# Kernel tuning notes

Hardware: AMD Instinct MI355X
Metric: run time of the kernel (lower is better)

The kernel has to match this reference:

```python
import jax, jax.numpy as jnp
import numpy as np

N, P, S, ENT = 256, 4, 40, 60
E = 1 + P + S + ENT          # 105 graph nodes (query + paras + sents + ents)
D = 1024                     # input_dim == hidden_dim
H, T = 8, 3                  # gnn heads, edge types
DH = D // H                  # per-head output dim
NEG = -1e30


def setup_inputs() -> dict:
    key = jax.random.key(0)
    ks = jax.random.split(key, 12)
    f = lambda k, sh, s: jax.random.normal(k, sh, jnp.float32) * s
    return {
        "query_vec": f(ks[0], (N, D), 1.0),
        "para_state": f(ks[1], (N, P, D), 1.0),
        "sent_state": f(ks[2], (N, S, D), 1.0),
        "ent_state": f(ks[3], (N, ENT, D), 1.0),
        "para_mask": jax.random.randint(ks[4], (N, P), 0, 2).astype(jnp.float32),
        "sent_mask": jax.random.randint(ks[5], (N, S), 0, 2).astype(jnp.float32),
        "ent_mask": jax.random.randint(ks[6], (N, ENT), 0, 2).astype(jnp.float32),
        "adj": jax.random.randint(ks[7], (N, E, E), 0, T + 1).astype(jnp.int32),
        "W": f(ks[8], (H, T, D, DH), 0.05),        # per head/edge-type projection
        "a": f(ks[9], (H, T, 2 * DH), 0.05),       # GAT attention vector [a1;a2]
        "qW1": f(ks[10], (H, T, D, 2 * DH), 0.05), # query-gate layer 1
        "qW2": f(ks[11], (H, T, 2 * DH, 2 * DH), 0.05),  # query-gate layer 2
    }


def _graph_block(x, query_vec, node_mask, adj, W, a, qW1, qW2):
    # x: [N,E,D], node_mask: [N,E,1], adj: [N,E,E] int (0 = no edge, 1..T = edge type)
    # per head/edge-type projections: [H,T,N,E,DH]
    h = jnp.einsum('ned,htdk->htnek', x, W)
    # query-conditioned gate (q_attn=True): sigmoid(relu(q @ W1) @ W2) -> [H,T,N,2DH]
    g = jax.nn.sigmoid(jnp.einsum('htnk,htkm->htnm',
                                  jax.nn.relu(jnp.einsum('nd,htdk->htnk', query_vec, qW1)),
                                  qW2))
    # decomposed GAT score: score[i,j] = lrelu((g1*h_i)@a1 + (g2*h_j)@a2)
    a1, a2 = a[..., :DH], a[..., DH:]
    f1 = jnp.einsum('htnek,htnk->htne', h, g[..., :DH] * a1[:, :, None, :])
    f2 = jnp.einsum('htnek,htnk->htne', h, g[..., DH:] * a2[:, :, None, :])
    score = jax.nn.leaky_relu(f1[..., :, None] + f2[..., None, :], 0.2)  # [H,T,N,E,E]
    # accumulate only where adj matches the edge type (i+1)
    etype = (jnp.arange(T, dtype=adj.dtype) + 1)[None, :, None, None, None]
    scores = jnp.sum(jnp.where(adj[None, None] == etype, score, 0.0), axis=1)  # [H,N,E,E]
    scores = jnp.where(adj[None] > 0, scores, NEG)
    coefs = jax.nn.softmax(scores, axis=-1)                 # [H,N,E,E]
    # original uses the last edge-type projection, node-masked, for aggregation
    h_last = h[:, -1] * node_mask[None]                     # [H,N,E,DH]
    out = jnp.einsum('hnij,hnjd->hnid', coefs, h_last)      # [H,N,E,DH]
    out = jnp.transpose(out, (1, 2, 0, 3)).reshape(x.shape[0], E, H * DH)
    out = jax.nn.relu(out)                                  # dropout p=0 in eval
    return out + x                                          # residual (identity align)


def reference(query_vec, para_state, sent_state, ent_state,
              para_mask, sent_mask, ent_mask, adj, W, a, qW1, qW2):
    x = jnp.concatenate([query_vec[:, None, :], para_state, sent_state, ent_state], axis=1)  # [N,E,D]
    node_mask = jnp.concatenate(
        [jnp.ones((x.shape[0], 1), x.dtype), para_mask, sent_mask, ent_mask], axis=-1)[..., None]  # [N,E,1]
    graph_state = _graph_block(x, query_vec, node_mask, adj, W, a, qW1, qW2)  # [N,E,D]
    return graph_state
```

## Files before the change

### kernel.cpp

```cpp
#include <hip/hip_runtime.h>
#include <stdint.h>


typedef unsigned short u16;
typedef __bf16 bf16;
typedef __bf16 bf16x8 __attribute__((ext_vector_type(8)));
typedef float f32x4 __attribute__((ext_vector_type(4)));

#define N_ 256
#define E_ 105
#define D_ 1024
#define H_ 8
#define DH_ 128
#define NE_ 26880

__device__ __forceinline__ u16 f2b(float f) { bf16 h = (bf16)f; return __builtin_bit_cast(u16, h); }
__device__ __forceinline__ float b2f(u16 u) { bf16 h = __builtin_bit_cast(bf16, u); return (float)h; }

#define AS1 __attribute__((address_space(1)))
#define AS3 __attribute__((address_space(3)))

__device__ __forceinline__ void load16_lds(const void* g, void* l) {
  __builtin_amdgcn_global_load_lds((AS1 void*)(unsigned long long)(uintptr_t)g,
                                   (AS3 void*)l, 16, 0, 0);
}

__device__ __forceinline__ void gemm128(u16* lds, const u16* A, const u16* B, int K,
                                        int lda, int ldb, f32x4 (&acc)[4][4]) {
  u16* lA = lds;
  u16* lB = lds + 8192;
  const int tid  = threadIdx.x;
  const int lane = tid & 63;
  const int wave = tid >> 6;
  const int ln15 = lane & 15;
  const int lq   = lane >> 4;
  const int wRow = (wave >> 1) * 64;
  const int wCol = (wave & 1) * 64;

  const int iters = K >> 6;
  for (int kt = 0; kt < iters; ++kt) {
    const char* Ab = (const char*)A + kt * 128;
    const char* Bb = (const char*)B + kt * 128;
#pragma unroll
    for (int m = 0; m < 4; ++m) {
      int ci  = m * 256 + tid;
      int row = ci >> 3;
      int g   = (ci & 7) ^ (row & 7);
      char* dstA = (char*)lA + m * 4096 + wave * 1024;
      char* dstB = (char*)lB + m * 4096 + wave * 1024;
      load16_lds(Ab + (long)row * ((long)lda * 2) + g * 16, dstA);
      load16_lds(Bb + (long)row * ((long)ldb * 2) + g * 16, dstB);
    }
    __syncthreads();
#pragma unroll
    for (int ks = 0; ks < 2; ++ks) {
      const int cc = ks * 4 + lq;
      bf16x8 af[4], bfv[4];
#pragma unroll
      for (int i = 0; i < 4; ++i) {
        int r = wRow + i * 16 + ln15;
        af[i] = *(const bf16x8*)&lA[r * 64 + ((cc ^ (r & 7)) << 3)];
        int c = wCol + i * 16 + ln15;
        bfv[i] = *(const bf16x8*)&lB[c * 64 + ((cc ^ (c & 7)) << 3)];
      }
#pragma unroll
      for (int i = 0; i < 4; ++i)
#pragma unroll
        for (int j = 0; j < 4; ++j)
          acc[i][j] = __builtin_amdgcn_mfma_f32_16x16x32_bf16(af[i], bfv[j], acc[i][j], 0, 0, 0);
    }
    __syncthreads();
  }
}

__device__ __forceinline__ void zero_acc(f32x4 (&acc)[4][4]) {
  f32x4 z = {0.f, 0.f, 0.f, 0.f};
#pragma unroll
  for (int i = 0; i < 4; ++i)
#pragma unroll
    for (int j = 0; j < 4; ++j) acc[i][j] = z;
}

__device__ __forceinline__ void tr_tile(const float* src, u16* dst, int R, int C,
                                        long sStr, long dStr, int bz, int bxy,
                                        u16 (*t)[33], int tid) {
  const int tilesC = C >> 5;
  const int tr = (bxy / tilesC) << 5;
  const int tc = (bxy % tilesC) << 5;
  const int lr = tid >> 5;
  const int lc = tid & 31;
#pragma unroll
  for (int i = 0; i < 4; ++i)
    t[lr + i * 8][lc] = f2b(src[bz * sStr + (long)(tr + lr + i * 8) * C + tc + lc]);
  __syncthreads();
#pragma unroll
  for (int i = 0; i < 4; ++i)
    dst[bz * dStr + (long)(tc + lr + i * 8) * R + tr + lc] = t[lc][lr + i * 8];
}

__global__ __launch_bounds__(256) void k_prep(const float* q, const float* para,
                                              const float* sent, const float* ent,
                                              const float* pm, const float* sm,
                                              const float* em, u16* x, float* nmask,
                                              const float* W, u16* Wb,
                                              const float* qW1, u16* qW1t,
                                              const float* qW2, u16* qW2t,
                                              u16* Wt) {
  __shared__ u16 t[32][33];
  const int b = blockIdx.x;
  const int tid = threadIdx.x;
  if (b < 13440) {
    long idx = (long)b * 256 + tid;
    int ne = (int)(idx >> 7), dc = (int)(idx & 127);
    int n = ne / E_, e = ne - n * E_;
    const float* src;
    if (e == 0)      src = q + (long)n * D_;
    else if (e < 5)  src = para + (long)(n * 4 + (e - 1)) * D_;
    else if (e < 45) src = sent + (long)(n * 40 + (e - 5)) * D_;
    else             src = ent + (long)(n * 60 + (e - 45)) * D_;
    float4 v0 = *(const float4*)(src + dc * 8);
    float4 v1 = *(const float4*)(src + dc * 8 + 4);
    uint4 o;
    o.x = (unsigned)f2b(v0.x) | ((unsigned)f2b(v0.y) << 16);
    o.y = (unsigned)f2b(v0.z) | ((unsigned)f2b(v0.w) << 16);
    o.z = (unsigned)f2b(v1.x) | ((unsigned)f2b(v1.y) << 16);
    o.w = (unsigned)f2b(v1.z) | ((unsigned)f2b(v1.w) << 16);
    *(uint4*)(x + (long)ne * D_ + dc * 8) = o;
    if (dc == 0) {
      float mv;
      if (e == 0)      mv = 1.f;
      else if (e < 5)  mv = pm[n * 4 + e - 1];
      else if (e < 45) mv = sm[n * 40 + e - 5];
      else             mv = em[n * 60 + e - 45];
      nmask[ne] = mv;
    }
  } else if (b < 16512) {
    long i = ((long)(b - 13440) * 256 + tid) * 4;
    float4 v = *(const float4*)(W + i);
    ushort4 o;
    o.x = f2b(v.x); o.y = f2b(v.y); o.z = f2b(v.z); o.w = f2b(v.w);
    *(ushort4*)(Wb + i) = o;
  } else if (b < 22656) {
    int idx = b - 16512;
    tr_tile(qW1, qW1t, 1024, 256, 262144, 262144, idx / 256, idx % 256, t, tid);
  } else if (b < 24192) {
    int idx = b - 22656;
    tr_tile(qW2, qW2t, 256, 256, 65536, 65536, idx / 64, idx % 64, t, tid);
  } else {
    int idx = b - 24192;
    tr_tile(W + 262144, Wt, 1024, 128, 393216, 131072, idx / 128, idx % 128, t, tid);
  }
}

__global__ __launch_bounds__(256) void k_qw1(const u16* x, const u16* qW1t, u16* r_bf) {
  __shared__ u16 shm[16384];
  const int bx = blockIdx.x;
  const int ht = bx >> 2, nt = (bx >> 1) & 1, mt = bx & 1;
  f32x4 acc[4][4];
  zero_acc(acc);
  gemm128(shm, x + (long)nt * 128 * (E_ * D_), qW1t + ((long)ht * 256 + mt * 128) * D_,
          1024, E_ * D_, 1024, acc);
  const int tid = threadIdx.x, lane = tid & 63, wave = tid >> 6;
  const int ln15 = lane & 15, lq = lane >> 4;
  const int wRow = (wave >> 1) * 64, wCol = (wave & 1) * 64;
#pragma unroll
  for (int rt = 0; rt < 4; ++rt)
#pragma unroll
    for (int ct = 0; ct < 4; ++ct)
#pragma unroll
      for (int rg = 0; rg < 4; ++rg) {
        int n = nt * 128 + wRow + rt * 16 + lq * 4 + rg;
        int m = mt * 128 + wCol + ct * 16 + ln15;
        float v = acc[rt][ct][rg];
        if (v < 0.f) v = 0.f;
        r_bf[((long)ht * 256 + n) * 256 + m] = f2b(v);
      }
}

__global__ __launch_bounds__(256) void k_qw2(const u16* r_bf, const u16* qW2t, const float* a,
                                             u16* ga) {
  __shared__ u16 shm[16384];
  const int bx = blockIdx.x;
  const int ht = bx >> 2, nt = (bx >> 1) & 1, mt = bx & 1;
  f32x4 acc[4][4];
  zero_acc(acc);
  gemm128(shm, r_bf + ((long)ht * 256 + nt * 128) * 256, qW2t + ((long)ht * 256 + mt * 128) * 256,
          256, 256, 256, acc);
  const int tid = threadIdx.x, lane = tid & 63, wave = tid >> 6;
  const int ln15 = lane & 15, lq = lane >> 4;
  const int wRow = (wave >> 1) * 64, wCol = (wave & 1) * 64;
#pragma unroll
  for (int rt = 0; rt < 4; ++rt)
#pragma unroll
    for (int ct = 0; ct < 4; ++ct)
#pragma unroll
      for (int rg = 0; rg < 4; ++rg) {
        int n = nt * 128 + wRow + rt * 16 + lq * 4 + rg;
        int m = mt * 128 + wCol + ct * 16 + ln15;
        float v = acc[rt][ct][rg];
        float sig = 1.f / (1.f + __expf(-v));
        float gv = sig * a[ht * 256 + m];
        int s = m >> 7, kk = m & 127;
        ga[(((long)ht * 2 + s) * 256 + n) * 128 + kk] = f2b(gv);
      }
}

__global__ __launch_bounds__(256) void k_w12(const u16* ga, const u16* Wb, u16* w12) {
  __shared__ u16 shm[16384];
  const int bx = blockIdx.x;
  const int c = bx >> 4, r2 = bx & 15;
  const int nt = r2 >> 3, dt = r2 & 7;
  const int ht = c >> 1;
  f32x4 acc[4][4];
  zero_acc(acc);
  gemm128(shm, ga + ((long)c * 256 + nt * 128) * 128, Wb + (long)ht * 131072 + dt * 128 * 128,
          128, 128, 128, acc);
  const int tid = threadIdx.x, lane = tid & 63, wave = tid >> 6;
  const int ln15 = lane & 15, lq = lane >> 4;
  const int wRow = (wave >> 1) * 64, wCol = (wave & 1) * 64;
#pragma unroll
  for (int rt = 0; rt < 4; ++rt)
#pragma unroll
    for (int ct = 0; ct < 4; ++ct)
#pragma unroll
      for (int rg = 0; rg < 4; ++rg) {
        int n = nt * 128 + wRow + rt * 16 + lq * 4 + rg;
        int d = dt * 128 + wCol + ct * 16 + ln15;
        w12[((long)n * 48 + c) * 1024 + d] = f2b(acc[rt][ct][rg]);
      }
}

__global__ __launch_bounds__(256) void k_f(const u16* x, const u16* w12, float* F) {
  __shared__ u16 shm[16384];
  const int n = blockIdx.x;
  f32x4 acc[4][4];
  zero_acc(acc);
  gemm128(shm, x + (long)n * E_ * D_, w12 + (long)n * 48 * 1024, 1024, 1024, 1024, acc);
  const int tid = threadIdx.x, lane = tid & 63, wave = tid >> 6;
  const int ln15 = lane & 15, lq = lane >> 4;
  const int wRow = (wave >> 1) * 64, wCol = (wave & 1) * 64;
#pragma unroll
  for (int rt = 0; rt < 4; ++rt)
#pragma unroll
    for (int ct = 0; ct < 4; ++ct)
#pragma unroll
      for (int rg = 0; rg < 4; ++rg) {
        int e = wRow + rt * 16 + lq * 4 + rg;
        int c = wCol + ct * 16 + ln15;
        if (e < 105 && c < 48) F[((long)n * 48 + c) * 105 + e] = acc[rt][ct][rg];
      }
}

__global__ __launch_bounds__(256) void k_h(const u16* x, const u16* Wt, const float* nmask,
                                           float* out) {
  __shared__ u16 shm[16384];
  const int bx = blockIdx.x;
  const int h = bx / 210;
  const int ne0 = (bx % 210) * 128;
  f32x4 acc[4][4];
  zero_acc(acc);
  gemm128(shm, x + (long)ne0 * D_, Wt + (long)h * DH_ * D_, 1024, 1024, 1024, acc);
  const int tid = threadIdx.x, lane = tid & 63, wave = tid >> 6;
  const int ln15 = lane & 15, lq = lane >> 4;
  const int wRow = (wave >> 1) * 64, wCol = (wave & 1) * 64;
#pragma unroll
  for (int rt = 0; rt < 4; ++rt)
#pragma unroll
    for (int ct = 0; ct < 4; ++ct)
#pragma unroll
      for (int rg = 0; rg < 4; ++rg) {
        int nel = wRow + rt * 16 + lq * 4 + rg;
        int k   = wCol + ct * 16 + ln15;
        shm[k * 128 + (nel ^ ((k & 15) << 3))] = f2b(acc[rt][ct][rg]);
      }
  __syncthreads();
  char* ob = (char*)out;
  const int nStart = ne0 / 105;
  const int nEnd   = (ne0 + 127) / 105;
  for (int n = nStart; n <= nEnd; ++n) {
    const long tb = (((long)n * 105) << 12) + ((long)h << 9);
    const int pe = n * 105 + 104;
    const bool ownPad = (pe >= ne0) && (pe < ne0 + 128);
    for (int t2 = tid; t2 < 14336; t2 += 256) {
      int c = t2 >> 10;
      int r = t2 & 1023;
      int k = r >> 3, e = r & 7;
      int j = c * 8 + e;
      int t = t2 * 2;
      long gb = tb + (long)(t >> 9) * 4096 + (t & 511);
      if (j < 105) {
        int ne = n * 105 + j;
        if (ne >= ne0 && ne < ne0 + 128) {
          int nel = ne - ne0;
          u16 v = shm[k * 128 + (nel ^ ((k & 15) << 3))];
          float mv = nmask[ne];
          *(u16*)(ob + gb) = (mv != 0.f) ? v : (u16)0;
        }
      } else if (ownPad) {
        *(u16*)(ob + gb) = 0;
      }
    }
  }
}

__global__ __launch_bounds__(256) void k_attn(const float* F, const int* adj, const u16* x,
                                              float* out) {
  const int h = blockIdx.x >> 8;
  const int n = blockIdx.x & 255;
  __shared__ u16 cb[112 * 128];
  __shared__ float f1s[3][112];
  __shared__ float f2s[3][112];
  const int tid = threadIdx.x;
  const int lane = tid & 63, wave = tid >> 6;

  for (int i = tid; i < 630; i += 256) {
    int t = i / 210;
    int rm = i - t * 210;
    int s = rm / 105;
    int e = rm - s * 105;
    float v = F[((long)n * 48 + (h * 3 + t) * 2 + s) * 105 + e];
    if (s == 0) f1s[t][e] = v; else f2s[t][e] = v;
  }
  {
    unsigned* cbz = (unsigned*)cb;
    for (int i = tid; i < 112 * 64; i += 256) cbz[i] = 0;
  }
  __syncthreads();

  {
    const int* abase = adj + (long)n * (E_ * E_);
    const int g  = lane >> 4;
    const int lg = lane & 15;
    float f2r[3][7];
#pragma unroll
    for (int m = 0; m < 7; ++m) {
      int j = lg + m * 16;
      bool jv = j < 105;
#pragma unroll
      for (int t = 0; t < 3; ++t) f2r[t][m] = jv ? f2s[t][j] : 0.f;
    }
    int avc[7];
    {
      int i0 = wave * 4 + g;
#pragma unroll
      for (int m = 0; m < 7; ++m) {
        int j = lg + m * 16;
        avc[m] = (j < 105) ? abase[i0 * E_ + j] : 0;
      }
    }
#pragma unroll
    for (int it = 0; it < 7; ++it) {
      int i = it * 16 + wave * 4 + g;
      bool iv = i < 105;
      int ir = iv ? i : 0;
      int avn[7];
      if (it < 6) {
        int in_ = i + 16;
        bool ivn = in_ < 105;
        int irn = ivn ? in_ : 0;
#pragma unroll
        for (int m = 0; m < 7; ++m) {
          int j = lg + m * 16;
          avn[m] = (ivn && j < 105) ? abase[irn * E_ + j] : 0;
        }
      }
      float f11 = f1s[0][ir], f12 = f1s[1][ir], f13 = f1s[2][ir];
      float s[7];
#pragma unroll
      for (int m = 0; m < 7; ++m) {
        int a_ = avc[m];
        float f1v = (a_ == 1) ? f11 : ((a_ == 2) ? f12 : f13);
        float f2v = (a_ == 1) ? f2r[0][m] : ((a_ == 2) ? f2r[1][m] : f2r[2][m]);
        float sv = f1v + f2v;
        sv = (sv < 0.f) ? 0.2f * sv : sv;
        s[m] = (a_ > 0) ? sv : -1e30f;
      }
      float mm = s[0];
#pragma unroll
      for (int m = 1; m < 7; ++m) mm = fmaxf(mm, s[m]);
#pragma unroll
      for (int d = 1; d < 16; d <<= 1) mm = fmaxf(mm, __shfl_xor(mm, d));
      float e[7];
      float sum = 0.f;
#pragma unroll
      for (int m = 0; m < 7; ++m) {
        int j = lg + m * 16;
        e[m] = (j < 105) ? __expf(s[m] - mm) : 0.f;
        sum += e[m];
      }
#pragma unroll
      for (int d = 1; d < 16; d <<= 1) sum += __shfl_xor(sum, d);
      float inv = 1.f / sum;
      if (iv) {
        const int rsw = i & 15;
#pragma unroll
        for (int m = 0; m < 7; ++m) {
          int j = lg + m * 16;
          if (j < 105)
            cb[i * 128 + ((((j >> 3) ^ rsw) << 3) + (j & 7))] = f2b(e[m] * inv);
        }
      }
      if (it < 6) {
#pragma unroll
        for (int m = 0; m < 7; ++m) avc[m] = avn[m];
      }
    }
  }
  __syncthreads();

  const char* hb = (const char*)out + (((long)n * 105) << 12) + ((long)h << 9);
  const int ln15 = lane & 15, lq = lane >> 4;
  const int nmt = (wave < 3) ? 2 : 1;
  f32x4 acc[2][8];
  {
    f32x4 z = {0.f, 0.f, 0.f, 0.f};
#pragma unroll
    for (int a_ = 0; a_ < 2; ++a_)
#pragma unroll
      for (int b_ = 0; b_ < 8; ++b_) acc[a_][b_] = z;
  }
#pragma unroll
  for (int ks = 0; ks < 4; ++ks) {
    const int cc = ks * 4 + lq;
    const int ccb = (cc < 14) ? cc : 0;
    bf16x8 bfr[8];
#pragma unroll
    for (int jn = 0; jn < 8; ++jn) {
      int k = jn * 16 + ln15;
      bfr[jn] = *(const bf16x8*)(hb + (long)(ccb * 4 + (k >> 5)) * 4096 + (k & 31) * 16);
    }
    __builtin_amdgcn_s_setprio(1);
#pragma unroll
    for (int im = 0; im < 2; ++im) {
      if (im < nmt) {
        int i = (wave + im * 4) * 16 + ln15;
        bf16x8 af = *(const bf16x8*)&cb[i * 128 + ((cc ^ (i & 15)) << 3)];
#pragma unroll
        for (int jn = 0; jn < 8; ++jn)
          acc[im][jn] = __builtin_amdgcn_mfma_f32_16x16x32_bf16(af, bfr[jn], acc[im][jn], 0, 0, 0);
      }
    }
    __builtin_amdgcn_s_setprio(0);
  }
  __syncthreads();

  float* sf = (float*)cb;
#pragma unroll
  for (int pass = 0; pass < 2; ++pass) {
    const int rbase = pass * 54;
    const int rcnt  = pass ? 51 : 54;
    for (int im = 0; im < nmt; ++im)
#pragma unroll
      for (int jn = 0; jn < 8; ++jn)
#pragma unroll
        for (int rg = 0; rg < 4; ++rg) {
          int i = (wave + im * 4) * 16 + lq * 4 + rg;
          if (i >= rbase && i < rbase + rcnt && i < 105) {
            int k = jn * 16 + ln15;
            float v = acc[im][jn][rg];
            sf[(i - rbase) * 132 + k] = v < 0.f ? 0.f : v;
          }
        }
    __syncthreads();
    for (int c = tid; c < rcnt * 32; c += 256) {
      int r = c >> 5, k4 = (c & 31) << 2;
      int i = rbase + r;
      float4 v = *(const float4*)&sf[r * 132 + k4];
      long xb = ((long)(n * E_ + i)) * D_ + h * DH_ + k4;
      ushort4 xv = *(const ushort4*)&x[xb];
      v.x += b2f(xv.x); v.y += b2f(xv.y); v.z += b2f(xv.z); v.w += b2f(xv.w);
      *(float4*)&out[xb] = v;
    }
    if (pass == 0) __syncthreads();
  }
}

extern "C" void kernel_launch(void* const* d_in, const int* in_sizes, int n_in,
                              void* d_out, int out_size, void* d_ws, size_t ws_size,
                              hipStream_t stream) {
  const float* q    = (const float*)d_in[0];
  const float* para = (const float*)d_in[1];
  const float* sent = (const float*)d_in[2];
  const float* ent  = (const float*)d_in[3];
  const float* pm   = (const float*)d_in[4];
  const float* sm   = (const float*)d_in[5];
  const float* em   = (const float*)d_in[6];
  const int*   adj  = (const int*)d_in[7];
  const float* W    = (const float*)d_in[8];
  const float* a    = (const float*)d_in[9];
  const float* qW1  = (const float*)d_in[10];
  const float* qW2  = (const float*)d_in[11];
  float* out = (float*)d_out;
  char* ws = (char*)d_ws;

  u16*   x     = (u16*)(ws);
  float* nmask = (float*)(ws + 55050240);
  u16*   Wb    = (u16*)(ws + 55682048);
  u16*   Wt    = (u16*)(ws + 61973504);
  u16*   qW1t  = (u16*)(ws + 64070656);
  u16*   qW2t  = (u16*)(ws + 76653568);
  u16*   r_bf  = (u16*)(ws + 79799296);
  u16*   ga    = (u16*)(ws + 82945024);
  u16*   w12   = (u16*)(ws + 86090752);
  float* F     = (float*)(ws + 111420416);

  k_prep<<<25216, 256, 0, stream>>>(q, para, sent, ent, pm, sm, em, x, nmask,
                                    W, Wb, qW1, qW1t, qW2, qW2t, Wt);
  k_qw1<<<96, 256, 0, stream>>>(x, qW1t, r_bf);
  k_qw2<<<96, 256, 0, stream>>>(r_bf, qW2t, a, ga);
  k_w12<<<768, 256, 0, stream>>>(ga, Wb, w12);
  k_f<<<256, 256, 0, stream>>>(x, w12, F);
  k_h<<<1680, 256, 0, stream>>>(x, Wt, nmask, out);
  k_attn<<<2048, 256, 0, stream>>>(F, adj, x, out);
}
```

Baseline: 678.8 us.

## Split prep kernel and write attention output directly from MFMA registers

Result: faster. 654.5 us (-3.6%).

```diff
diff --git a/kernel.cpp b/kernel.cpp
--- a/kernel.cpp
+++ b/kernel.cpp
@@ -81,14 +81,55 @@
     for (int j = 0; j < 4; ++j) acc[i][j] = z;
 }
 
-__device__ __forceinline__ void tr_tile(const float* src, u16* dst, int R, int C,
-                                        long sStr, long dStr, int bz, int bxy,
-                                        u16 (*t)[33], int tid) {
+__global__ __launch_bounds__(256) void k_cast(const float* src, u16* dst, long n) {
+  long i = ((long)blockIdx.x * 256 + threadIdx.x) * 4;
+  if (i >= n) return;
+  float4 v = *(const float4*)(src + i);
+  ushort4 o;
+  o.x = f2b(v.x); o.y = f2b(v.y); o.z = f2b(v.z); o.w = f2b(v.w);
+  *(ushort4*)(dst + i) = o;
+}
+
+__global__ __launch_bounds__(256) void k_build(const float* q, const float* para,
+                                               const float* sent, const float* ent,
+                                               const float* pm, const float* sm,
+                                               const float* em, u16* x, float* nmask) {
+  long idx = (long)blockIdx.x * 256 + threadIdx.x;
+  if (idx >= (long)NE_ * 128) return;
+  int ne = (int)(idx >> 7), dc = (int)(idx & 127);
+  int n = ne / E_, e = ne - n * E_;
+  const float* src;
+  if (e == 0)      src = q + (long)n * D_;
+  else if (e < 5)  src = para + (long)(n * 4 + (e - 1)) * D_;
+  else if (e < 45) src = sent + (long)(n * 40 + (e - 5)) * D_;
+  else             src = ent + (long)(n * 60 + (e - 45)) * D_;
+  float4 v0 = *(const float4*)(src + dc * 8);
+  float4 v1 = *(const float4*)(src + dc * 8 + 4);
+  uint4 o;
+  o.x = (unsigned)f2b(v0.x) | ((unsigned)f2b(v0.y) << 16);
+  o.y = (unsigned)f2b(v0.z) | ((unsigned)f2b(v0.w) << 16);
+  o.z = (unsigned)f2b(v1.x) | ((unsigned)f2b(v1.y) << 16);
+  o.w = (unsigned)f2b(v1.z) | ((unsigned)f2b(v1.w) << 16);
+  *(uint4*)(x + (long)ne * D_ + dc * 8) = o;
+  if (dc == 0) {
+    float mv;
+    if (e == 0)      mv = 1.f;
+    else if (e < 5)  mv = pm[n * 4 + e - 1];
+    else if (e < 45) mv = sm[n * 40 + e - 5];
+    else             mv = em[n * 60 + e - 45];
+    nmask[ne] = mv;
+  }
+}
+
+__global__ __launch_bounds__(256) void k_tr(const float* src, u16* dst, int R, int C,
+                                            long sStr, long dStr) {
+  __shared__ u16 t[32][33];
+  const int bz = blockIdx.y;
   const int tilesC = C >> 5;
-  const int tr = (bxy / tilesC) << 5;
-  const int tc = (bxy % tilesC) << 5;
-  const int lr = tid >> 5;
-  const int lc = tid & 31;
+  const int tr = (blockIdx.x / tilesC) << 5;
+  const int tc = (blockIdx.x % tilesC) << 5;
+  const int lr = threadIdx.x >> 5;
+  const int lc = threadIdx.x & 31;
 #pragma unroll
   for (int i = 0; i < 4; ++i)
     t[lr + i * 8][lc] = f2b(src[bz * sStr + (long)(tr + lr + i * 8) * C + tc + lc]);
@@ -96,60 +137,6 @@
 #pragma unroll
   for (int i = 0; i < 4; ++i)
     dst[bz * dStr + (long)(tc + lr + i * 8) * R + tr + lc] = t[lc][lr + i * 8];
-}
-
-__global__ __launch_bounds__(256) void k_prep(const float* q, const float* para,
-                                              const float* sent, const float* ent,
-                                              const float* pm, const float* sm,
-                                              const float* em, u16* x, float* nmask,
-                                              const float* W, u16* Wb,
-                                              const float* qW1, u16* qW1t,
-                                              const float* qW2, u16* qW2t,
-                                              u16* Wt) {
-  __shared__ u16 t[32][33];
-  const int b = blockIdx.x;
-  const int tid = threadIdx.x;
-  if (b < 13440) {
-    long idx = (long)b * 256 + tid;
-    int ne = (int)(idx >> 7), dc = (int)(idx & 127);
-    int n = ne / E_, e = ne - n * E_;
-    const float* src;
-    if (e == 0)      src = q + (long)n * D_;
-    else if (e < 5)  src = para + (long)(n * 4 + (e - 1)) * D_;
-    else if (e < 45) src = sent + (long)(n * 40 + (e - 5)) * D_;
-    else             src = ent + (long)(n * 60 + (e - 45)) * D_;
-    float4 v0 = *(const float4*)(src + dc * 8);
-    float4 v1 = *(const float4*)(src + dc * 8 + 4);
-    uint4 o;
-    o.x = (unsigned)f2b(v0.x) | ((unsigned)f2b(v0.y) << 16);
-    o.y = (unsigned)f2b(v0.z) | ((unsigned)f2b(v0.w) << 16);
-    o.z = (unsigned)f2b(v1.x) | ((unsigned)f2b(v1.y) << 16);
-    o.w = (unsigned)f2b(v1.z) | ((unsigned)f2b(v1.w) << 16);
-    *(uint4*)(x + (long)ne * D_ + dc * 8) = o;
-    if (dc == 0) {
-      float mv;
-      if (e == 0)      mv = 1.f;
-      else if (e < 5)  mv = pm[n * 4 + e - 1];
-      else if (e < 45) mv = sm[n * 40 + e - 5];
-      else             mv = em[n * 60 + e - 45];
-      nmask[ne] = mv;
-    }
-  } else if (b < 16512) {
-    long i = ((long)(b - 13440) * 256 + tid) * 4;
-    float4 v = *(const float4*)(W + i);
-    ushort4 o;
-    o.x = f2b(v.x); o.y = f2b(v.y); o.z = f2b(v.z); o.w = f2b(v.w);
-    *(ushort4*)(Wb + i) = o;
-  } else if (b < 22656) {
-    int idx = b - 16512;
-    tr_tile(qW1, qW1t, 1024, 256, 262144, 262144, idx / 256, idx % 256, t, tid);
-  } else if (b < 24192) {
-    int idx = b - 22656;
-    tr_tile(qW2, qW2t, 256, 256, 65536, 65536, idx / 64, idx % 64, t, tid);
-  } else {
-    int idx = b - 24192;
-    tr_tile(W + 262144, Wt, 1024, 128, 393216, 131072, idx / 128, idx % 128, t, tid);
-  }
 }
 
 __global__ __launch_bounds__(256) void k_qw1(const u16* x, const u16* qW1t, u16* r_bf) {
@@ -321,9 +308,11 @@
     float v = F[((long)n * 48 + (h * 3 + t) * 2 + s) * 105 + e];
     if (s == 0) f1s[t][e] = v; else f2s[t][e] = v;
   }
-  {
-    unsigned* cbz = (unsigned*)cb;
-    for (int i = tid; i < 112 * 64; i += 256) cbz[i] = 0;
+  for (int idx = tid; idx < 1680; idx += 256) {
+    int i = idx >> 4, sl = idx & 15;
+    int rsw = i & 15;
+    int pos = (((14 + (sl >> 3)) ^ rsw) << 3) + (sl & 7);
+    cb[i * 128 + pos] = 0;
   }
   __syncthreads();
 
@@ -396,8 +385,7 @@
 #pragma unroll
         for (int m = 0; m < 7; ++m) {
           int j = lg + m * 16;
-          if (j < 105)
-            cb[i * 128 + ((((j >> 3) ^ rsw) << 3) + (j & 7))] = f2b(e[m] * inv);
+          cb[i * 128 + ((((j >> 3) ^ rsw) << 3) + (j & 7))] = f2b(e[m] * inv);
         }
       }
       if (it < 6) {
@@ -437,41 +425,32 @@
         bf16x8 af = *(const bf16x8*)&cb[i * 128 + ((cc ^ (i & 15)) << 3)];
 #pragma unroll
         for (int jn = 0; jn < 8; ++jn)
-          acc[im][jn] = __builtin_amdgcn_mfma_f32_16x16x32_bf16(af, bfr[jn], acc[im][jn], 0, 0, 0);
+          acc[im][jn] = __builtin_amdgcn_mfma_f32_16x16x32_bf16(bfr[jn], af, acc[im][jn], 0, 0, 0);
       }
     }
     __builtin_amdgcn_s_setprio(0);
   }
   __syncthreads();
 
-  float* sf = (float*)cb;
-#pragma unroll
-  for (int pass = 0; pass < 2; ++pass) {
-    const int rbase = pass * 54;
-    const int rcnt  = pass ? 51 : 54;
-    for (int im = 0; im < nmt; ++im)
-#pragma unroll
-      for (int jn = 0; jn < 8; ++jn)
-#pragma unroll
-        for (int rg = 0; rg < 4; ++rg) {
-          int i = (wave + im * 4) * 16 + lq * 4 + rg;
-          if (i >= rbase && i < rbase + rcnt && i < 105) {
-            int k = jn * 16 + ln15;
-            float v = acc[im][jn][rg];
-            sf[(i - rbase) * 132 + k] = v < 0.f ? 0.f : v;
-          }
-        }
-    __syncthreads();
-    for (int c = tid; c < rcnt * 32; c += 256) {
-      int r = c >> 5, k4 = (c & 31) << 2;
-      int i = rbase + r;
-      float4 v = *(const float4*)&sf[r * 132 + k4];
-      long xb = ((long)(n * E_ + i)) * D_ + h * DH_ + k4;
-      ushort4 xv = *(const ushort4*)&x[xb];
-      v.x += b2f(xv.x); v.y += b2f(xv.y); v.z += b2f(xv.z); v.w += b2f(xv.w);
-      *(float4*)&out[xb] = v;
-    }
-    if (pass == 0) __syncthreads();
+  for (int im = 0; im < nmt; ++im) {
+    int i = (wave + im * 4) * 16 + ln15;
+    if (i < 105) {
+      long rb = ((long)(n * E_ + i)) * D_ + h * DH_ + lq * 4;
+#pragma unroll
+      for (int jn = 0; jn < 8; ++jn) {
+        f32x4 v = acc[im][jn];
+#pragma unroll
+        for (int c = 0; c < 4; ++c) v[c] = v[c] < 0.f ? 0.f : v[c];
+        long xb = rb + jn * 16;
+        ushort4 xv = *(const ushort4*)&x[xb];
+        float4 o;
+        o.x = v[0] + b2f(xv.x);
+        o.y = v[1] + b2f(xv.y);
+        o.z = v[2] + b2f(xv.z);
+        o.w = v[3] + b2f(xv.w);
+        *(float4*)&out[xb] = o;
+      }
+    }
   }
 }
 
@@ -504,8 +483,11 @@
   u16*   w12   = (u16*)(ws + 86090752);
   float* F     = (float*)(ws + 111420416);
 
-  k_prep<<<25216, 256, 0, stream>>>(q, para, sent, ent, pm, sm, em, x, nmask,
-                                    W, Wb, qW1, qW1t, qW2, qW2t, Wt);
+  k_build<<<13440, 256, 0, stream>>>(q, para, sent, ent, pm, sm, em, x, nmask);
+  k_cast<<<3072, 256, 0, stream>>>(W, Wb, 3145728);
+  k_tr<<<dim3(256, 24), 256, 0, stream>>>(qW1, qW1t, 1024, 256, 262144, 262144);
+  k_tr<<<dim3(64, 24), 256, 0, stream>>>(qW2, qW2t, 256, 256, 65536, 65536);
+  k_tr<<<dim3(128, 8), 256, 0, stream>>>(W + 262144, Wt, 1024, 128, 393216, 131072);
   k_qw1<<<96, 256, 0, stream>>>(x, qW1t, r_bf);
   k_qw2<<<96, 256, 0, stream>>>(r_bf, qW2t, a, ga);
   k_w12<<<768, 256, 0, stream>>>(ga, Wb, w12);
```
